# Optimization experiments

Hardware: AMD Instinct MI355X
Metric: run time of the kernel (lower is better)

The kernel has to match this reference:

```python
import jax, jax.numpy as jnp
import numpy as np

EPS = 1e-6
NUM_HEADS = 8
HEAD_DIM = 64
ROPE_BASE = 100.0


def _rope_cos_sin(dim, height, width, base=ROPE_BASE):
    quarter = dim // 4
    inv_freq = 1.0 / (base ** (jnp.arange(quarter, dtype=jnp.float32) / quarter))
    freqs_y = jnp.arange(height, dtype=jnp.float32)[:, None] * inv_freq  # (H, q)
    emb_y = jnp.concatenate([freqs_y, freqs_y], axis=-1)                 # (H, dim//2)
    freqs_x = jnp.arange(width, dtype=jnp.float32)[:, None] * inv_freq
    emb_x = jnp.concatenate([freqs_x, freqs_x], axis=-1)                 # (W, dim//2)
    emb_y_grid = jnp.broadcast_to(emb_y[:, None, :], (height, width, dim // 2))
    emb_x_grid = jnp.broadcast_to(emb_x[None, :, :], (height, width, dim // 2))
    full = jnp.concatenate([emb_y_grid, emb_x_grid], axis=-1).reshape(-1, dim)  # (H*W, dim)
    return jnp.cos(full), jnp.sin(full)


def _rotate_half(x):
    x1, x2 = jnp.split(x, 2, axis=-1)
    return jnp.concatenate([-x2, x1], axis=-1)


def setup_inputs() -> dict:
    key = jax.random.key(0)
    ks = jax.random.split(key, 8)
    B, C, H, W = 16, 512, 32, 32
    t_dim = 512
    inner = NUM_HEADS * HEAD_DIM  # 512
    s = 0.02
    return {
        "x": jax.random.normal(ks[0], (B, C, H, W), dtype=jnp.float32),
        "time_emb": jax.random.normal(ks[1], (B, t_dim), dtype=jnp.float32),
        "tm_w1": jax.random.normal(ks[2], (t_dim, t_dim), dtype=jnp.float32) * s,
        "tm_b1": jnp.zeros((t_dim,), dtype=jnp.float32),
        "tm_w2": jax.random.normal(ks[3], (t_dim, 2 * C), dtype=jnp.float32) * s,
        "tm_b2": jnp.zeros((2 * C,), dtype=jnp.float32),
        "qkv_w": jax.random.normal(ks[4], (C, 3 * inner), dtype=jnp.float32) * s,
        "out_w": jax.random.normal(ks[5], (inner, C), dtype=jnp.float32) * s,
        "out_b": jnp.zeros((C,), dtype=jnp.float32),
    }


def reference(x, time_emb, tm_w1, tm_b1, tm_w2, tm_b2, qkv_w, out_w, out_b):
    B, C, H, W = x.shape
    N = H * W
    h, d = NUM_HEADS, HEAD_DIM

    # AdaCLN: channel-wise layernorm with time-conditioned affine modulation
    u = jnp.mean(x, axis=1, keepdims=True)
    s = jnp.mean((x - u) ** 2, axis=1, keepdims=True)
    x_norm = (x - u) / jnp.sqrt(s + EPS)
    emb = jax.nn.silu(time_emb @ tm_w1 + tm_b1) @ tm_w2 + tm_b2  # (B, 2C)
    gamma, beta = jnp.split(emb, 2, axis=1)
    x_norm = x_norm * (1.0 + gamma[:, :, None, None]) + beta[:, :, None, None]

    # (B, C, H, W) -> (B, N, C)
    tokens = x_norm.transpose(0, 2, 3, 1).reshape(B, N, C)

    qkv = tokens @ qkv_w  # (B, N, 3*inner)
    q, k, v = jnp.split(qkv, 3, axis=-1)
    q = q.reshape(B, N, h, d).transpose(0, 2, 1, 3)  # (B, h, N, d)
    k = k.reshape(B, N, h, d).transpose(0, 2, 1, 3)
    v = v.reshape(B, N, h, d).transpose(0, 2, 1, 3)

    cos, sin = _rope_cos_sin(d, H, W)  # (N, d)
    q = q * cos + _rotate_half(q) * sin
    k = k * cos + _rotate_half(k) * sin

    # SDPA, scale = 1/sqrt(head_dim)
    scale = 1.0 / jnp.sqrt(jnp.asarray(d, dtype=q.dtype))
    scores = jnp.einsum("bhqd,bhkd->bhqk", q, k) * scale
    attn = jax.nn.softmax(scores, axis=-1)
    out = jnp.einsum("bhqk,bhkd->bhqd", attn, v)  # (B, h, N, d)

    out = out.transpose(0, 2, 1, 3).reshape(B, N, h * d)
    out = out @ out_w + out_b  # (B, N, C)
    out = out.reshape(B, H, W, C).transpose(0, 3, 1, 2)
    return x + out
```

## Files before the change

### kernel.cpp

```cpp
#include <hip/hip_runtime.h>
#include <stdint.h>
#include <stddef.h>

#define B_  16
#define C_  512
#define N_  1024
#define NH  8
#define HD  64

typedef __attribute__((ext_vector_type(8))) short bf16x8;
typedef __attribute__((ext_vector_type(4))) float f32x4;
typedef __attribute__((ext_vector_type(2))) __bf16 bf16x2t;
typedef __attribute__((ext_vector_type(2))) unsigned uint2v;

__device__ __forceinline__ float bf2f(short s) {
    unsigned u = ((unsigned)(unsigned short)s) << 16;
    return __builtin_bit_cast(float, u);
}
__device__ __forceinline__ unsigned packcvt(float lo, float hi) {
    bf16x2t v = { (__bf16)lo, (__bf16)hi };
    return __builtin_bit_cast(unsigned, v);
}
__device__ __forceinline__ short f2bf_hw(float f) {
    __bf16 b = (__bf16)f;
    return __builtin_bit_cast(short, b);
}
__device__ __forceinline__ float fexp2(float x) {
#if __has_builtin(__builtin_amdgcn_exp2f)
    return __builtin_amdgcn_exp2f(x);
#else
    return exp2f(x);
#endif
}
__device__ __forceinline__ void plswap32(unsigned& a, unsigned& b) {
#if __has_builtin(__builtin_amdgcn_permlane32_swap)
    uint2v r = __builtin_amdgcn_permlane32_swap(a, b, false, false);
    a = r.x; b = r.y;
#else
    unsigned ax = (unsigned)__shfl_xor((int)a, 32, 64), bx = (unsigned)__shfl_xor((int)b, 32, 64);
    bool hi = (threadIdx.x & 32) != 0;
    unsigned na = hi ? bx : a, nb = hi ? b : ax;
    a = na; b = nb;
#endif
}
__device__ __forceinline__ void plswap16(unsigned& a, unsigned& b) {
#if __has_builtin(__builtin_amdgcn_permlane16_swap)
    uint2v r = __builtin_amdgcn_permlane16_swap(a, b, false, false);
    a = r.x; b = r.y;
#else
    unsigned ax = (unsigned)__shfl_xor((int)a, 16, 64), bx = (unsigned)__shfl_xor((int)b, 16, 64);
    bool hi = (threadIdx.x & 16) != 0;
    unsigned na = hi ? bx : a, nb = hi ? b : ax;
    a = na; b = nb;
#endif
}
__device__ __forceinline__ float bcf(unsigned u) { return __builtin_bit_cast(float, u); }
__device__ __forceinline__ unsigned bcu(float f) { return __builtin_bit_cast(unsigned, f); }
__device__ __forceinline__ float redsum_lg(float x) {
    unsigned a = bcu(x), b = a; plswap32(a, b);
    float s = bcf(a) + bcf(b);
    a = bcu(s); b = a; plswap16(a, b);
    return bcf(a) + bcf(b);
}

#define MFMA16(a, b, c) __builtin_amdgcn_mfma_f32_16x16x32_bf16((a), (b), (c), 0, 0, 0)

typedef __attribute__((address_space(3))) unsigned int lds_u32;
typedef __attribute__((address_space(1))) unsigned int glb_u32;
__device__ __forceinline__ void gload16(const void* g, void* l) {
    __builtin_amdgcn_global_load_lds((const glb_u32*)g, (lds_u32*)l, 16, 0, 0);
}

__global__ __launch_bounds__(256) void k_prep(
        const float* __restrict__ qkv_w, const float* __restrict__ out_w,
        short* __restrict__ qkvwT, short* __restrict__ outwT,
        float4* __restrict__ ropetab) {
    int bid = blockIdx.x, tid = threadIdx.x;
    if (bid < 256) {
        const float* src; short* dst; int J, jt, kt;
        if (bid < 192) { src = qkv_w; dst = qkvwT; J = 1536; jt = (bid % 24) * 64; kt = (bid / 24) * 64; }
        else { int b2 = bid - 192; src = out_w; dst = outwT; J = 512; jt = (b2 & 7) * 64; kt = (b2 >> 3) * 64; }
        __shared__ float ts[64][65];
        int r = tid >> 4, c4 = (tid & 15) * 4;
        for (int rr = 0; rr < 64; rr += 16) {
            float4 v = *(const float4*)(src + (size_t)(kt + rr + r) * J + jt + c4);
            ts[c4 + 0][rr + r] = v.x;
            ts[c4 + 1][rr + r] = v.y;
            ts[c4 + 2][rr + r] = v.z;
            ts[c4 + 3][rr + r] = v.w;
        }
        __syncthreads();
        int jr = tid >> 2, kc = (tid & 3) * 16;
        unsigned w[8];
#pragma unroll
        for (int i = 0; i < 8; i++) w[i] = packcvt(ts[jr][kc + 2 * i], ts[jr][kc + 2 * i + 1]);
        short* dp = dst + (size_t)(jt + jr) * 512 + kt + kc;
        *(uint4*)(dp)     = make_uint4(w[0], w[1], w[2], w[3]);
        *(uint4*)(dp + 8) = make_uint4(w[4], w[5], w[6], w[7]);
    } else {
        int idx = (bid - 256) * 256 + tid;
        int n = idx >> 5, dq = idx & 31, i = dq & 15;
        float w = powf(100.0f, -(float)i * (1.0f / 16.0f));
        float y = (float)(n >> 5), xx = (float)(n & 31);
        ropetab[idx] = make_float4(cosf(y * w), sinf(y * w), cosf(xx * w), sinf(xx * w));
    }
}

__global__ __launch_bounds__(256) void k_mlp1(
        const float* __restrict__ temb, const float* __restrict__ w1, const float* __restrict__ b1,
        float* __restrict__ h) {
    int b = blockIdx.y, jt = blockIdx.x, tid = threadIdx.x;
    int jl = tid & 31, j = jt * 32 + jl, ks = tid >> 5;
    __shared__ float tl[512];
    __shared__ float ps[8][32];
    tl[tid] = temb[b * 512 + tid];
    tl[tid + 256] = temb[b * 512 + tid + 256];
    __syncthreads();
    float acc = 0.f;
    const float* wp = w1 + (size_t)(ks * 64) * 512 + j;
#pragma unroll 8
    for (int kk = 0; kk < 64; kk++) acc += tl[ks * 64 + kk] * wp[(size_t)kk * 512];
    ps[ks][jl] = acc;
    __syncthreads();
    if (tid < 32) {
        float s = ((ps[0][tid] + ps[1][tid]) + (ps[2][tid] + ps[3][tid]))
                + ((ps[4][tid] + ps[5][tid]) + (ps[6][tid] + ps[7][tid]));
        s += b1[jt * 32 + tid];
        h[b * 512 + jt * 32 + tid] = s / (1.0f + __expf(-s));
    }
}

__global__ __launch_bounds__(256) void k_mlp2(
        const float* __restrict__ h, const float* __restrict__ w2, const float* __restrict__ b2,
        float* __restrict__ gbout) {
    int b = blockIdx.y, jt = blockIdx.x, tid = threadIdx.x;
    int jl = tid & 31, j = jt * 32 + jl, ks = tid >> 5;
    __shared__ float hl[512];
    __shared__ float ps[8][32];
    hl[tid] = h[b * 512 + tid];
    hl[tid + 256] = h[b * 512 + tid + 256];
    __syncthreads();
    float acc = 0.f;
    const float* wp = w2 + (size_t)(ks * 64) * 1024 + j;
#pragma unroll 8
    for (int kk = 0; kk < 64; kk++) acc += hl[ks * 64 + kk] * wp[(size_t)kk * 1024];
    ps[ks][jl] = acc;
    __syncthreads();
    if (tid < 32) {
        float s = ((ps[0][tid] + ps[1][tid]) + (ps[2][tid] + ps[3][tid]))
                + ((ps[4][tid] + ps[5][tid]) + (ps[6][tid] + ps[7][tid]));
        gbout[b * 1024 + jt * 32 + tid] = s + b2[jt * 32 + tid];
    }
}

__global__ __launch_bounds__(256) void k_adacln(
        const float* __restrict__ x, const float* __restrict__ gb, short* __restrict__ tokens) {
    int b = blockIdx.y, n0 = blockIdx.x * 64;
    int tid = threadIdx.x;
    const float* xb = x + (size_t)b * C_ * N_;
    __shared__ float4 rs4[16][16], rq4[16][16];
    __shared__ float mean_s[64], rstd_s[64];
    __shared__ float xs[64][65];

    {
        int q = tid & 15, s = tid >> 4;
        float4 sum = make_float4(0.f, 0.f, 0.f, 0.f);
        float4 sq  = make_float4(0.f, 0.f, 0.f, 0.f);
        const float* xp = xb + (size_t)(s * 32) * N_ + n0 + q * 4;
#pragma unroll 8
        for (int ci = 0; ci < 32; ci++) {
            float4 v = *(const float4*)(xp + (size_t)ci * N_);
            sum.x += v.x; sum.y += v.y; sum.z += v.z; sum.w += v.w;
            sq.x += v.x * v.x; sq.y += v.y * v.y; sq.z += v.z * v.z; sq.w += v.w * v.w;
        }
        rs4[s][q] = sum; rq4[s][q] = sq;
    }
    __syncthreads();
    if (tid < 64) {
        int q = tid >> 2, j = tid & 3;
        float s1 = 0.f, s2 = 0.f;
#pragma unroll
        for (int s = 0; s < 16; s++) {
            float4 a = rs4[s][q], c = rq4[s][q];
            s1 += (&a.x)[j];
            s2 += (&c.x)[j];
        }
        float mu = s1 * (1.0f / 512.0f);
        float var = s2 * (1.0f / 512.0f) - mu * mu;
        mean_s[tid] = mu;
        rstd_s[tid] = rsqrtf(var + 1e-6f);
    }
    const float* gam = gb + b * 1024;
    const float* bet = gam + 512;
    int ch = tid & 7;
    for (int ct = 0; ct < 8; ct++) {
        __syncthreads();
#pragma unroll
        for (int itr = 0; itr < 4; itr++) {
            int cl = itr * 16 + (tid >> 4), q = tid & 15;
            float4 v = *(const float4*)(xb + (size_t)(ct * 64 + cl) * N_ + n0 + q * 4);
            xs[cl][q * 4 + 0] = v.x;
            xs[cl][q * 4 + 1] = v.y;
            xs[cl][q * 4 + 2] = v.z;
            xs[cl][q * 4 + 3] = v.w;
        }
        __syncthreads();
#pragma unroll
        for (int pp = 0; pp < 2; pp++) {
            int p = pp * 32 + (tid >> 3);
            float mu = mean_s[p], rt = rstd_s[p];
            float v[8];
#pragma unroll
            for (int j = 0; j < 8; j++) {
                int c = ct * 64 + ch * 8 + j;
                v[j] = (xs[ch * 8 + j][p] - mu) * rt * (1.0f + gam[c]) + bet[c];
            }
            uint4 ov = make_uint4(packcvt(v[0], v[1]), packcvt(v[2], v[3]),
                                  packcvt(v[4], v[5]), packcvt(v[6], v[7]));
            *(uint4*)(tokens + ((size_t)(b * N_ + n0 + p)) * C_ + ct * 64 + ch * 8) = ov;
        }
    }
}

__global__ __launch_bounds__(256) void k_gemm_qkv(
        const short* __restrict__ A, const short* __restrict__ Bt,
        const float4* __restrict__ ropetab,
        short* __restrict__ qr, short* __restrict__ kr, short* __restrict__ vt) {
    __shared__ short Asm[128 * 32];
    __shared__ short Bsm[128 * 32];
    int wgid = blockIdx.x;
    int orig = (wgid & 7) * 192 + (wgid >> 3);
    int bx = orig % 12, by = orig / 12;
    int tid = threadIdx.x, wv = tid >> 6, ln = tid & 63;
    int wr = wv >> 1, wc = wv & 1, lr = ln & 15, lg = ln >> 4;
    const short* Ab = A + (size_t)by * 128 * 512;
    const short* Bb = Bt + (size_t)bx * 128 * 512;
    f32x4 acc[4][4] = {};
    int srow = ln >> 2, sch = ln & 3;
    for (int kb = 0; kb < 512; kb += 32) {
        int r0 = wv * 32;
        const short* ga = Ab + (size_t)(r0 + srow) * 512 + kb + sch * 8;
        gload16(ga, (void*)(Asm + r0 * 32));
        gload16(ga + 16 * 512, (void*)(Asm + (r0 + 16) * 32));
        const short* gbp = Bb + (size_t)(r0 + srow) * 512 + kb + sch * 8;
        gload16(gbp, (void*)(Bsm + r0 * 32));
        gload16(gbp + 16 * 512, (void*)(Bsm + (r0 + 16) * 32));
        __syncthreads();
        bf16x8 af[4], bfr[4];
#pragma unroll
        for (int m = 0; m < 4; m++) af[m] = *(const bf16x8*)(Asm + (wr * 64 + m * 16 + lr) * 32 + lg * 8);
#pragma unroll
        for (int f = 0; f < 4; f++) bfr[f] = *(const bf16x8*)(Bsm + (wc * 64 + f * 16 + lr) * 32 + lg * 8);
#pragma unroll
        for (int m = 0; m < 4; m++)
#pragma unroll
            for (int f = 0; f < 4; f++)
                acc[m][f] = MFMA16(af[m], bfr[f], acc[m][f]);
        __syncthreads();
    }
    int mbase = by * 128;
    int sec = bx >> 2;
    int h = (2 * bx + wc) & 7;
    if (sec < 2) {
        short* dst0 = (sec == 0) ? qr : kr;
#pragma unroll
        for (int m = 0; m < 4; m++) {
            int gmb = mbase + wr * 64 + m * 16 + lg * 4;
#pragma unroll
            for (int r = 0; r < 4; r++) {
                int gm = gmb + r; int b = gm >> 10, n = gm & 1023;
                short* rowp = dst0 + (((size_t)b * NH + h) * N_ + n) * HD;
                const float4* tr = ropetab + n * 32;
#pragma unroll
                for (int f2 = 0; f2 < 2; f2++) {
                    int d_lo = f2 * 16 + lr;
                    float4 t = tr[d_lo];
                    float a = acc[m][f2][r], bb2 = acc[m][f2 + 2][r];
                    rowp[d_lo]      = f2bf_hw(a * t.x - bb2 * t.y);
                    rowp[d_lo + 32] = f2bf_hw(bb2 * t.z + a * t.w);
                }
            }
        }
    } else {
#pragma unroll
        for (int m = 0; m < 4; m++) {
            int gmb = mbase + wr * 64 + m * 16 + lg * 4;
            int b = gmb >> 10, n0 = gmb & 1023;
#pragma unroll
            for (int f = 0; f < 4; f++) {
                int d = f * 16 + lr;
                uint2 val;
                val.x = packcvt(acc[m][f][0], acc[m][f][1]);
                val.y = packcvt(acc[m][f][2], acc[m][f][3]);
                *(uint2*)(vt + (((size_t)b * NH + h) * HD + d) * N_ + n0) = val;
            }
        }
    }
}

__global__ __launch_bounds__(512) void k_flash10(
        const short* __restrict__ qr, const short* __restrict__ kr, const short* __restrict__ vt,
        short* __restrict__ attn_out) {
    __shared__ short Ks[3][4096];
    __shared__ short Vs[3][4096];
    int bh = blockIdx.x, b = bh >> 3, h = bh & 7;
    int qt = blockIdx.y;
    int tid = threadIdx.x, wv = tid >> 6, ln = tid & 63;
    int lr = ln & 15, lg = ln >> 4;
    int qhalf = wv >> 2, w4 = wv & 3;
    const short* Qb = qr + ((size_t)bh * N_ + qt * 256 + qhalf * 128 + w4 * 32) * HD;
    const short* Kb = kr + (size_t)bh * N_ * HD;
    const short* Vb = vt + (size_t)bh * HD * N_;

    const float QSCALE = 0.125f * 1.44269504f;
    bf16x8 qf[2][2];
#pragma unroll
    for (int qg = 0; qg < 2; qg++)
#pragma unroll
        for (int hf = 0; hf < 2; hf++) {
            bf16x8 raw = *(const bf16x8*)(Qb + (qg * 16 + lr) * 64 + hf * 32 + lg * 8);
            bf16x8 sc;
#pragma unroll
            for (int j = 0; j < 8; j++) sc[j] = f2bf_hw(bf2f(raw[j]) * QSCALE);
            qf[qg][hf] = sc;
        }

    int srow = ln >> 3, cpos = ln & 7;
    int rloc = wv * 8 + srow;
    int csrc = cpos ^ (srow & 7);

    float l_part[2] = {0.f, 0.f};
    f32x4 ao[2][4] = {};

    asm volatile("s_waitcnt vmcnt(0)" ::: "memory");
    __builtin_amdgcn_sched_barrier(0);

#pragma unroll
    for (int t0 = 0; t0 < 2; t0++) {
        gload16(Kb + ((size_t)(t0 * 64 + rloc)) * 64 + csrc * 8,
                (void*)&Ks[t0][rloc * 64]);
        gload16(Vb + ((size_t)rloc) * 1024 + t0 * 64 + csrc * 8,
                (void*)&Vs[t0][rloc * 64]);
    }
    asm volatile("s_waitcnt vmcnt(2)" ::: "memory");
    __builtin_amdgcn_s_barrier();
    __builtin_amdgcn_sched_barrier(0);

    for (int kt = 0; kt < 16; kt++) {
        int cur = kt % 3;
        if (kt < 14) {
            int nxt = (kt + 2) % 3, ktn = kt + 2;
            gload16(Kb + ((size_t)(ktn * 64 + rloc)) * 64 + csrc * 8,
                    (void*)&Ks[nxt][rloc * 64]);
            gload16(Vb + ((size_t)rloc) * 1024 + ktn * 64 + csrc * 8,
                    (void*)&Vs[nxt][rloc * 64]);
        }

        f32x4 sT[2][4];
#pragma unroll
        for (int f = 0; f < 4; f++) {
            int r = f * 16 + lr;
            const short* kp = &Ks[cur][r * 64];
            bf16x8 ka  = *(const bf16x8*)(kp + ((lg ^ (r & 7)) * 8));
            bf16x8 kb2 = *(const bf16x8*)(kp + (((4 + lg) ^ (r & 7)) * 8));
#pragma unroll
            for (int qg = 0; qg < 2; qg++) {
                f32x4 s = {};
                s = MFMA16(ka, qf[qg][0], s);
                s = MFMA16(kb2, qf[qg][1], s);
                sT[qg][f] = s;
            }
        }

        union U4 { unsigned u[4]; bf16x8 v; };
        U4 pb[2][2];
#pragma unroll
        for (int qg = 0; qg < 2; qg++) {
            float rsum = 0.f;
            unsigned pk[4][2];
#pragma unroll
            for (int f = 0; f < 4; f++) {
                float p0 = fexp2(sT[qg][f][0]);
                float p1 = fexp2(sT[qg][f][1]);
                float p2 = fexp2(sT[qg][f][2]);
                float p3 = fexp2(sT[qg][f][3]);
                rsum += (p0 + p1) + (p2 + p3);
                pk[f][0] = packcvt(p0, p1);
                pk[f][1] = packcvt(p2, p3);
            }
            l_part[qg] += rsum;

#pragma unroll
            for (int kb = 0; kb < 2; kb++) {
                unsigned a = pk[2 * kb][0], c = pk[2 * kb + 1][0];
                plswap32(a, c); plswap16(a, c);
                pb[qg][kb].u[0] = a; pb[qg][kb].u[2] = c;
                unsigned bb = pk[2 * kb][1], d = pk[2 * kb + 1][1];
                plswap32(bb, d); plswap16(bb, d);
                pb[qg][kb].u[1] = bb; pb[qg][kb].u[3] = d;
            }
        }

#pragma unroll
        for (int dt = 0; dt < 4; dt++) {
            int rr = dt * 16 + lr;
            const short* vp = &Vs[cur][rr * 64];
            bf16x8 va0 = *(const bf16x8*)(vp + ((lg ^ (rr & 7)) * 8));
            bf16x8 va1 = *(const bf16x8*)(vp + (((4 + lg) ^ (rr & 7)) * 8));
#pragma unroll
            for (int qg = 0; qg < 2; qg++) {
                ao[qg][dt] = MFMA16(va0, pb[qg][0].v, ao[qg][dt]);
                ao[qg][dt] = MFMA16(va1, pb[qg][1].v, ao[qg][dt]);
            }
        }

        if (kt < 15) {
            if (kt < 14) asm volatile("s_waitcnt vmcnt(2)" ::: "memory");
            else         asm volatile("s_waitcnt vmcnt(0)" ::: "memory");
            __builtin_amdgcn_s_barrier();
            __builtin_amdgcn_sched_barrier(0);
        }
    }

#pragma unroll
    for (int qg = 0; qg < 2; qg++) {
        float inv = 1.0f / redsum_lg(l_part[qg]);
        int qglob = qt * 256 + qhalf * 128 + w4 * 32 + qg * 16 + lr;
        size_t ob = ((size_t)b * N_ + qglob) * 512 + h * 64 + lg * 4;
#pragma unroll
        for (int dt = 0; dt < 4; dt++) {
            uint2 val;
            val.x = packcvt(ao[qg][dt][0] * inv, ao[qg][dt][1] * inv);
            val.y = packcvt(ao[qg][dt][2] * inv, ao[qg][dt][3] * inv);
            *(uint2*)(attn_out + ob + dt * 16) = val;
        }
    }
}

__global__ __launch_bounds__(256) void k_gemm_out(
        const short* __restrict__ A, const short* __restrict__ Bt,
        const float* __restrict__ x, const float* __restrict__ obias, float* __restrict__ out) {
    __shared__ short Asm[128 * 32];
    __shared__ short Bsm[128 * 32];
    int tid = threadIdx.x, wv = tid >> 6, ln = tid & 63;
    int wr = wv >> 1, wc = wv & 1, lr = ln & 15, lg = ln >> 4;
    const short* Ab = A + (size_t)blockIdx.y * 128 * 512;
    const short* Bb = Bt + (size_t)blockIdx.x * 128 * 512;
    f32x4 acc[4][4] = {};
    int srow = ln >> 2, sch = ln & 3;
    for (int kb = 0; kb < 512; kb += 32) {
        int r0 = wv * 32;
        const short* ga = Ab + (size_t)(r0 + srow) * 512 + kb + sch * 8;
        gload16(ga, (void*)(Asm + r0 * 32));
        gload16(ga + 16 * 512, (void*)(Asm + (r0 + 16) * 32));
        const short* gbp = Bb + (size_t)(r0 + srow) * 512 + kb + sch * 8;
        gload16(gbp, (void*)(Bsm + r0 * 32));
        gload16(gbp + 16 * 512, (void*)(Bsm + (r0 + 16) * 32));
        __syncthreads();
        bf16x8 af[4], bfr[4];
#pragma unroll
        for (int m = 0; m < 4; m++) af[m] = *(const bf16x8*)(Asm + (wr * 64 + m * 16 + lr) * 32 + lg * 8);
#pragma unroll
        for (int f = 0; f < 4; f++) bfr[f] = *(const bf16x8*)(Bsm + (wc * 64 + f * 16 + lr) * 32 + lg * 8);
#pragma unroll
        for (int m = 0; m < 4; m++)
#pragma unroll
            for (int f = 0; f < 4; f++)
                acc[m][f] = MFMA16(af[m], bfr[f], acc[m][f]);
        __syncthreads();
    }
    int cb = blockIdx.y * 128 + wr * 64, tb = blockIdx.x * 128 + wc * 64;
#pragma unroll
    for (int m = 0; m < 4; m++) {
#pragma unroll
        for (int f = 0; f < 4; f++) {
            int gt = tb + f * 16 + lr;
            int b = gt >> 10, n = gt & 1023;
#pragma unroll
            for (int r = 0; r < 4; r++) {
                int gc = cb + m * 16 + lg * 4 + r;
                size_t ad = ((size_t)b * C_ + gc) * N_ + n;
                out[ad] = acc[m][f][r] + obias[gc] + x[ad];
            }
        }
    }
}

extern "C" void kernel_launch(void* const* d_in, const int* in_sizes, int n_in,
                              void* d_out, int out_size, void* d_ws, size_t ws_size,
                              hipStream_t stream) {
    const float* x     = (const float*)d_in[0];
    const float* temb  = (const float*)d_in[1];
    const float* tm_w1 = (const float*)d_in[2];
    const float* tm_b1 = (const float*)d_in[3];
    const float* tm_w2 = (const float*)d_in[4];
    const float* tm_b2 = (const float*)d_in[5];
    const float* qkv_w = (const float*)d_in[6];
    const float* out_w = (const float*)d_in[7];
    const float* out_b = (const float*)d_in[8];
    float* out = (float*)d_out;

    char* ws = (char*)d_ws;
    short*  qkvwT  = (short*)(ws);
    short*  outwT  = (short*)(ws + 1572864);
    float4* ropetab= (float4*)(ws + 2097152);
    float*  gb     = (float*)(ws + 2621440);
    short*  tokens = (short*)(ws + 2686976);
    short*  qr     = (short*)(ws + 19464192);
    short*  kr     = (short*)(ws + 36241408);
    short*  vt     = (short*)(ws + 53018624);
    short*  attn   = tokens;
    float*  hbuf   = (float*)(ws + 2686976);

    k_prep<<<dim3(384), dim3(256), 0, stream>>>(qkv_w, out_w, qkvwT, outwT, ropetab);
    k_mlp1<<<dim3(16, 16), dim3(256), 0, stream>>>(temb, tm_w1, tm_b1, hbuf);
    k_mlp2<<<dim3(32, 16), dim3(256), 0, stream>>>(hbuf, tm_w2, tm_b2, gb);
    k_adacln<<<dim3(16, 16), dim3(256), 0, stream>>>(x, gb, tokens);
    k_gemm_qkv<<<dim3(1536), dim3(256), 0, stream>>>(tokens, qkvwT, ropetab, qr, kr, vt);
    k_flash10<<<dim3(128, 4), dim3(512), 0, stream>>>(qr, kr, vt, attn);
    k_gemm_out<<<dim3(128, 4), dim3(256), 0, stream>>>(outwT, attn, x, out_b, out);
}
```

Measured before the change: 148.4 us.

## Double-buffer LDS tiles in QKV and output-projection GEMMs

Both projection GEMMs now keep two LDS buffers for the A and B tiles. The next K-slice is issued with direct-to-LDS global loads while MFMAs run on the current slice. This is meant to hide global load latency behind compute and remove one of the two barriers per iteration. In exchange, LDS use per block doubles to 32 KB, which could limit occupancy. Correctness depends on the async LDS loads being properly fenced by the remaining barrier and vmcnt waits.

```diff
diff --git a/kernel.cpp b/kernel.cpp
--- a/kernel.cpp
+++ b/kernel.cpp
@@ -226,8 +226,8 @@
         const short* __restrict__ A, const short* __restrict__ Bt,
         const float4* __restrict__ ropetab,
         short* __restrict__ qr, short* __restrict__ kr, short* __restrict__ vt) {
-    __shared__ short Asm[128 * 32];
-    __shared__ short Bsm[128 * 32];
+    __shared__ short Asm[2][4096];
+    __shared__ short Bsm[2][4096];
     int wgid = blockIdx.x;
     int orig = (wgid & 7) * 192 + (wgid >> 3);
     int bx = orig % 12, by = orig / 12;
@@ -237,20 +237,34 @@
     const short* Bb = Bt + (size_t)bx * 128 * 512;
     f32x4 acc[4][4] = {};
     int srow = ln >> 2, sch = ln & 3;
-    for (int kb = 0; kb < 512; kb += 32) {
-        int r0 = wv * 32;
-        const short* ga = Ab + (size_t)(r0 + srow) * 512 + kb + sch * 8;
-        gload16(ga, (void*)(Asm + r0 * 32));
-        gload16(ga + 16 * 512, (void*)(Asm + (r0 + 16) * 32));
-        const short* gbp = Bb + (size_t)(r0 + srow) * 512 + kb + sch * 8;
-        gload16(gbp, (void*)(Bsm + r0 * 32));
-        gload16(gbp + 16 * 512, (void*)(Bsm + (r0 + 16) * 32));
-        __syncthreads();
+    int r0 = wv * 32;
+
+    {
+        const short* ga = Ab + (size_t)(r0 + srow) * 512 + sch * 8;
+        gload16(ga, (void*)(&Asm[0][r0 * 32]));
+        gload16(ga + 16 * 512, (void*)(&Asm[0][(r0 + 16) * 32]));
+        const short* gbp = Bb + (size_t)(r0 + srow) * 512 + sch * 8;
+        gload16(gbp, (void*)(&Bsm[0][r0 * 32]));
+        gload16(gbp + 16 * 512, (void*)(&Bsm[0][(r0 + 16) * 32]));
+    }
+    __syncthreads();
+
+    for (int kt = 0; kt < 16; kt++) {
+        int cur = kt & 1;
+        if (kt < 15) {
+            int nxt = cur ^ 1, kb = (kt + 1) * 32;
+            const short* ga = Ab + (size_t)(r0 + srow) * 512 + kb + sch * 8;
+            gload16(ga, (void*)(&Asm[nxt][r0 * 32]));
+            gload16(ga + 16 * 512, (void*)(&Asm[nxt][(r0 + 16) * 32]));
+            const short* gbp = Bb + (size_t)(r0 + srow) * 512 + kb + sch * 8;
+            gload16(gbp, (void*)(&Bsm[nxt][r0 * 32]));
+            gload16(gbp + 16 * 512, (void*)(&Bsm[nxt][(r0 + 16) * 32]));
+        }
         bf16x8 af[4], bfr[4];
 #pragma unroll
-        for (int m = 0; m < 4; m++) af[m] = *(const bf16x8*)(Asm + (wr * 64 + m * 16 + lr) * 32 + lg * 8);
-#pragma unroll
-        for (int f = 0; f < 4; f++) bfr[f] = *(const bf16x8*)(Bsm + (wc * 64 + f * 16 + lr) * 32 + lg * 8);
+        for (int m = 0; m < 4; m++) af[m] = *(const bf16x8*)(&Asm[cur][(wr * 64 + m * 16 + lr) * 32 + lg * 8]);
+#pragma unroll
+        for (int f = 0; f < 4; f++) bfr[f] = *(const bf16x8*)(&Bsm[cur][(wc * 64 + f * 16 + lr) * 32 + lg * 8]);
 #pragma unroll
         for (int m = 0; m < 4; m++)
 #pragma unroll
@@ -440,28 +454,42 @@
 __global__ __launch_bounds__(256) void k_gemm_out(
         const short* __restrict__ A, const short* __restrict__ Bt,
         const float* __restrict__ x, const float* __restrict__ obias, float* __restrict__ out) {
-    __shared__ short Asm[128 * 32];
-    __shared__ short Bsm[128 * 32];
+    __shared__ short Asm[2][4096];
+    __shared__ short Bsm[2][4096];
     int tid = threadIdx.x, wv = tid >> 6, ln = tid & 63;
     int wr = wv >> 1, wc = wv & 1, lr = ln & 15, lg = ln >> 4;
     const short* Ab = A + (size_t)blockIdx.y * 128 * 512;
     const short* Bb = Bt + (size_t)blockIdx.x * 128 * 512;
     f32x4 acc[4][4] = {};
     int srow = ln >> 2, sch = ln & 3;
-    for (int kb = 0; kb < 512; kb += 32) {
-        int r0 = wv * 32;
-        const short* ga = Ab + (size_t)(r0 + srow) * 512 + kb + sch * 8;
-        gload16(ga, (void*)(Asm + r0 * 32));
-        gload16(ga + 16 * 512, (void*)(Asm + (r0 + 16) * 32));
-        const short* gbp = Bb + (size_t)(r0 + srow) * 512 + kb + sch * 8;
-        gload16(gbp, (void*)(Bsm + r0 * 32));
-        gload16(gbp + 16 * 512, (void*)(Bsm + (r0 + 16) * 32));
-        __syncthreads();
+    int r0 = wv * 32;
+
+    {
+        const short* ga = Ab + (size_t)(r0 + srow) * 512 + sch * 8;
+        gload16(ga, (void*)(&Asm[0][r0 * 32]));
+        gload16(ga + 16 * 512, (void*)(&Asm[0][(r0 + 16) * 32]));
+        const short* gbp = Bb + (size_t)(r0 + srow) * 512 + sch * 8;
+        gload16(gbp, (void*)(&Bsm[0][r0 * 32]));
+        gload16(gbp + 16 * 512, (void*)(&Bsm[0][(r0 + 16) * 32]));
+    }
+    __syncthreads();
+
+    for (int kt = 0; kt < 16; kt++) {
+        int cur = kt & 1;
+        if (kt < 15) {
+            int nxt = cur ^ 1, kb = (kt + 1) * 32;
+            const short* ga = Ab + (size_t)(r0 + srow) * 512 + kb + sch * 8;
+            gload16(ga, (void*)(&Asm[nxt][r0 * 32]));
+            gload16(ga + 16 * 512, (void*)(&Asm[nxt][(r0 + 16) * 32]));
+            const short* gbp = Bb + (size_t)(r0 + srow) * 512 + kb + sch * 8;
+            gload16(gbp, (void*)(&Bsm[nxt][r0 * 32]));
+            gload16(gbp + 16 * 512, (void*)(&Bsm[nxt][(r0 + 16) * 32]));
+        }
         bf16x8 af[4], bfr[4];
 #pragma unroll
-        for (int m = 0; m < 4; m++) af[m] = *(const bf16x8*)(Asm + (wr * 64 + m * 16 + lr) * 32 + lg * 8);
-#pragma unroll
-        for (int f = 0; f < 4; f++) bfr[f] = *(const bf16x8*)(Bsm + (wc * 64 + f * 16 + lr) * 32 + lg * 8);
+        for (int m = 0; m < 4; m++) af[m] = *(const bf16x8*)(&Asm[cur][(wr * 64 + m * 16 + lr) * 32 + lg * 8]);
+#pragma unroll
+        for (int f = 0; f < 4; f++) bfr[f] = *(const bf16x8*)(&Bsm[cur][(wc * 64 + f * 16 + lr) * 32 + lg * 8]);
 #pragma unroll
         for (int m = 0; m < 4; m++)
 #pragma unroll
```

Measured after the change: 160.3 us. +8.0%, slower.
